# Kernel tuning notes

Hardware: AMD Instinct MI355X
Metric: run time of the kernel (lower is better)

The kernel has to match this reference:

```python
import jax, jax.numpy as jnp
import numpy as np


def _resize_axis(x, axis, n_out):
    # trilinear (per-axis linear) resize, matching torch align_corners=False
    n_in = x.shape[axis]
    coords = jnp.clip((jnp.arange(n_out) + 0.5) * (n_in / n_out) - 0.5, 0.0, n_in - 1)
    lo = jnp.floor(coords).astype(jnp.int32)
    hi = jnp.minimum(lo + 1, n_in - 1)
    w = (coords - lo).astype(x.dtype)
    shp = [1] * x.ndim
    shp[axis] = n_out
    w = w.reshape(shp)
    return jnp.take(x, lo, axis=axis) * (1 - w) + jnp.take(x, hi, axis=axis) * w


def setup_inputs() -> dict:
    key = jax.random.key(0)
    ks = jax.random.split(key, 16)
    M, B, C, H, W, Z = 4, 1, 64, 64, 64, 64
    mini = max(C // 32, 4)  # = 4
    s = 0.05
    return {
        'modalities': jax.random.normal(ks[0], (M, B, C, H, W, Z), jnp.float32),
        'wq1': jax.random.normal(ks[1], (mini, C), jnp.float32) * s,
        'bq1': jax.random.normal(ks[2], (mini,), jnp.float32) * s,
        'wq2': jax.random.normal(ks[3], (2, mini), jnp.float32) * s,
        'bq2': jax.random.normal(ks[4], (2,), jnp.float32) * s,
        'wa1': jax.random.normal(ks[5], (mini, C), jnp.float32) * s,
        'ba1': jax.random.normal(ks[6], (mini,), jnp.float32) * s,
        'wa2': jax.random.normal(ks[7], (1, mini), jnp.float32) * s,
        'ba2': jax.random.normal(ks[8], (1,), jnp.float32) * s,
        'wf': jax.random.normal(ks[9], (C, C), jnp.float32) * s,
        'bf': jax.random.normal(ks[10], (C,), jnp.float32) * s,
        'wg1': jax.random.normal(ks[11], (mini, C), jnp.float32) * s,
        'bg1': jax.random.normal(ks[12], (mini,), jnp.float32) * s,
        'wg2': jax.random.normal(ks[13], (C, mini), jnp.float32) * s,
        'bg2': jax.random.normal(ks[14], (C,), jnp.float32) * s,
    }


def reference(modalities, wq1, bq1, wq2, bq2, wa1, ba1, wa2, ba2, wf, bf, wg1, bg1, wg2, bg2):
    M, B, C, H, W, Z = modalities.shape
    x = modalities
    # quality net: GAP -> 1x1 conv -> relu -> 1x1 conv -> sigmoid (all 1x1x1 convs == matmuls)
    gap = x.mean(axis=(3, 4, 5))  # [M,B,C]
    scores = jax.nn.sigmoid(jnp.maximum(gap @ wq1.T + bq1, 0.0) @ wq2.T + bq2)  # [M,B,2]
    qw = scores.mean(axis=2)      # quality_weight per modality, [M,B] (mean over ch+unit spatial)
    t = qw.mean(axis=1)           # scalar weight contribution per modality, [M]
    # cross attention: adaptive avg pool to 4^3, tiny MLP, trilinear upsample back to H,W,Z
    d = x.reshape(M, B, C, 4, H // 4, 4, W // 4, 4, Z // 4).mean(axis=(4, 6, 8))  # [M,B,C,4,4,4]
    h = jnp.maximum(jnp.einsum('mbcxyz,kc->mbkxyz', d, wa1) + ba1.reshape(1, 1, -1, 1, 1, 1), 0.0)
    a = jax.nn.sigmoid(jnp.einsum('mbkxyz,ok->mboxyz', h, wa2) + ba2.reshape(1, 1, -1, 1, 1, 1))
    a = _resize_axis(_resize_axis(_resize_axis(a, 3, H), 4, W), 5, Z)  # [M,B,1,H,W,Z]
    # pairwise aggregation: enhancement_i = sum_{j!=i} x_j * attn_j * qw_j, normalized by sum_{j!=i} t_j
    contrib = x * a * qw[:, :, None, None, None, None]  # [M,B,C,H,W,Z]
    S = contrib.sum(axis=0, keepdims=True)
    T = t.sum()
    enh = (S - contrib) / (T - t)[:, None, None, None, None, None]
    # fusion 1x1 conv + gate
    fused = jnp.einsum('mbchwz,dc->mbdhwz', enh, wf) + bf.reshape(1, 1, -1, 1, 1, 1)
    g = fused.mean(axis=(3, 4, 5))  # [M,B,C]
    gate = jax.nn.sigmoid(jnp.maximum(g @ wg1.T + bg1, 0.0) @ wg2.T + bg2)  # [M,B,C]
    enhanced = x + gate[:, :, :, None, None, None] * fused
    boundary = scores[:, :, 0].reshape(M, B, 1, 1, 1, 1)
    semantic = scores[:, :, 1].reshape(M, B, 1, 1, 1, 1)
    return enhanced, boundary, semantic
```

## Files before the change

### kernel.cpp

```cpp
#include <hip/hip_runtime.h>
#include <math.h>

typedef __attribute__((ext_vector_type(4))) float f4;
typedef __attribute__((ext_vector_type(8))) short s8v;
typedef __attribute__((ext_vector_type(4))) unsigned int u4v;
typedef __attribute__((ext_vector_type(2))) unsigned int u2v;

#define NVOX 262144
#define MB_TOT 67108864

__device__ __forceinline__ float sigm(float x){ return 1.0f/(1.0f+expf(-x)); }
__device__ __forceinline__ unsigned short f2b(float f){
  unsigned x = __float_as_uint(f);
  return (unsigned short)((x + 0x7fffu + ((x>>16)&1u)) >> 16);
}
__device__ __forceinline__ unsigned cvtpk(float lo, float hi){
  unsigned r;
  asm("v_cvt_pk_bf16_f32 %0, %1, %2" : "=v"(r) : "v"(lo), "v"(hi));
  return r;
}
__device__ __forceinline__ float bl(unsigned u){ return __uint_as_float(u<<16); }
__device__ __forceinline__ float bh(unsigned u){ return __uint_as_float(u & 0xffff0000u); }


#define LD(I,J) (*reinterpret_cast<const f4*>(xp + (size_t)((I)*64 + (J))*64 + chunk*4))

#define BODY(I, V) { \
  float s_ = ((V).x+(V).y)+((V).z+(V).w); \
  float wB_ = (V).x*wqz0 + (V).y*wqz1 + (V).z*wqz2 + (V).w*wqz3; \
  float wA_ = s_ - wB_; \
  bacc += s_; \
  const int   li_  = ((I)<8)?0:(((I)>=56)?3:(((I)-8)>>4)); \
  const float wi_  = ((I)<8||(I)>=56)?0.0f:(((I)+0.5f)*0.0625f-0.5f-(float)li_); \
  const float h0_ = (li_==0)?(1.0f-wi_):0.0f; \
  const float h1_ = (li_==1)?(1.0f-wi_):((li_==0)?wi_:0.0f); \
  const float h2_ = (li_==2)?(1.0f-wi_):((li_==1)?wi_:0.0f); \
  const float h3_ = (li_==3)?(1.0f-wi_):((li_==2)?wi_:0.0f); \
  float eA_ = cjA*wA_, eB_ = cjA*wB_, fA_ = cjB*wA_, fB_ = cjB*wB_; \
  if (h0_ != 0.0f){ a0A0 += h0_*eA_; a0A1 += h0_*eB_; a0B0 += h0_*fA_; a0B1 += h0_*fB_; } \
  if (h1_ != 0.0f){ a1A0 += h1_*eA_; a1A1 += h1_*eB_; a1B0 += h1_*fA_; a1B1 += h1_*fB_; } \
  if (h2_ != 0.0f){ a2A0 += h2_*eA_; a2A1 += h2_*eB_; a2B0 += h2_*fA_; a2B1 += h2_*fB_; } \
  if (h3_ != 0.0f){ a3A0 += h3_*eA_; a3A1 += h3_*eB_; a3B0 += h3_*fA_; a3B1 += h3_*fB_; } \
}

#define SEG16(I0) \
  _Pragma("unroll") \
  for (int ib=0; ib<16; ib+=4){ \
    f4 v0_ = LD((I0)+ib+0, j); \
    f4 v1_ = LD((I0)+ib+1, j); \
    f4 v2_ = LD((I0)+ib+2, j); \
    f4 v3_ = LD((I0)+ib+3, j); \
    BODY((I0)+ib+0, v0_); \
    BODY((I0)+ib+1, v1_); \
    BODY((I0)+ib+2, v2_); \
    BODY((I0)+ib+3, v3_); \
  }

__global__ __launch_bounds__(512) void k_pass1(const float* __restrict__ x,
                                               float* __restrict__ dsums,
                                               float* __restrict__ xbsums){
  __shared__ float xbL[64];
  __shared__ float bsL[64];
  int tid = threadIdx.x;
  int b = blockIdx.x;
  int mc  = b >> 2;
  int seg = b & 3;
  if (tid < 64){ xbL[tid]=0.f; bsL[tid]=0.f; }
  __syncthreads();
  const float* xp = x + (size_t)mc * NVOX;
  int chunk = tid & 15;
  int jbase = tid >> 4;
  float wqz0,wqz1,wqz2,wqz3;
  {
    int z0 = chunk*4;
    int lzc0 = (z0<8)?0:((z0>=56)?3:((z0-8)>>4));
    wqz0 = (z0  <8||z0  >=56)?0.0f:((z0+0.5f)*0.0625f-0.5f-(float)lzc0);
    wqz1 = (z0+1<8||z0+1>=56)?0.0f:((z0+1.5f)*0.0625f-0.5f-(float)lzc0);
    wqz2 = (z0+2<8||z0+2>=56)?0.0f:((z0+2.5f)*0.0625f-0.5f-(float)lzc0);
    wqz3 = (z0+3<8||z0+3>=56)?0.0f:((z0+3.5f)*0.0625f-0.5f-(float)lzc0);
  }
  int lzc = (chunk*4<8)?0:((chunk*4>=56)?3:((chunk*4-8)>>4));
  int kq = chunk >> 2;

#pragma unroll
  for (int jh=0; jh<2; ++jh){
    int j = jbase + jh*32;
    float cjA, cjB; int lj;
    {
      float cj = fminf(fmaxf((j+0.5f)*0.0625f-0.5f, 0.0f), 3.0f);
      lj = (int)cj; float wj = cj - (float)lj;
      cjA = 1.0f - wj; cjB = wj;
    }
    float a0A0=0.f,a0A1=0.f,a0B0=0.f,a0B1=0.f;
    float a1A0=0.f,a1A1=0.f,a1B0=0.f,a1B1=0.f;
    float a2A0=0.f,a2A1=0.f,a2B0=0.f,a2B1=0.f;
    float a3A0=0.f,a3A1=0.f,a3B0=0.f,a3B1=0.f;
    float bacc=0.f;

    if      (seg == 0){ SEG16(0)  }
    else if (seg == 1){ SEG16(16) }
    else if (seg == 2){ SEG16(32) }
    else              { SEG16(48) }

    {
      int p00 = lj*4 + lzc;
      atomicAdd(&xbL[ 0 + p00], a0A0);
      atomicAdd(&xbL[16 + p00], a1A0);
      atomicAdd(&xbL[32 + p00], a2A0);
      atomicAdd(&xbL[48 + p00], a3A0);
      if (lzc < 3){
        atomicAdd(&xbL[ 0 + p00+1], a0A1);
        atomicAdd(&xbL[16 + p00+1], a1A1);
        atomicAdd(&xbL[32 + p00+1], a2A1);
        atomicAdd(&xbL[48 + p00+1], a3A1);
      }
      if (lj < 3){
        atomicAdd(&xbL[ 0 + p00+4], a0B0);
        atomicAdd(&xbL[16 + p00+4], a1B0);
        atomicAdd(&xbL[32 + p00+4], a2B0);
        atomicAdd(&xbL[48 + p00+4], a3B0);
        if (lzc < 3){
          atomicAdd(&xbL[ 0 + p00+5], a0B1);
          atomicAdd(&xbL[16 + p00+5], a1B1);
          atomicAdd(&xbL[32 + p00+5], a2B1);
          atomicAdd(&xbL[48 + p00+5], a3B1);
        }
      }
      atomicAdd(&bsL[seg*16 + (j>>4)*4 + kq], bacc);
    }
  }
  __syncthreads();
  if (tid < 64){
    atomicAdd(&xbsums[(size_t)mc*64 + tid], xbL[tid]);
    atomicAdd(&dsums [(size_t)mc*64 + tid], bsL[tid]);
  }
}

__global__ __launch_bounds__(256) void k_pass2(
    const float* __restrict__ dsums, const float* __restrict__ xbsums,
    const float* __restrict__ wq1, const float* __restrict__ bq1,
    const float* __restrict__ wq2, const float* __restrict__ bq2,
    const float* __restrict__ wa1, const float* __restrict__ ba1,
    const float* __restrict__ wa2, const float* __restrict__ ba2,
    const float* __restrict__ wf,  const float* __restrict__ bfv,
    const float* __restrict__ wg1, const float* __restrict__ bg1,
    const float* __restrict__ wg2, const float* __restrict__ bg2,
    float* __restrict__ wsa, float* __restrict__ wsgate,
    float* __restrict__ wsqw, float* __restrict__ wsinv,
    unsigned short* __restrict__ wfb,
    float* __restrict__ outp)
{
  __shared__ float sGap[256];
  __shared__ float sA[256];
  __shared__ float sCm[256];
  __shared__ float sG[256];
  __shared__ float sGG[16];
  __shared__ float sQw[4];
  int tid = threadIdx.x;
  int m = tid>>6, c = tid&63;
  for (int t = tid; t < 4096; t += 256) wfb[t] = f2b(wf[t]);
  {
    float s=0.f;
    const float* dp = dsums + (size_t)tid*64;
    for (int p=0;p<64;++p) s += dp[p];
    sGap[tid] = s * (1.0f/262144.0f);
  }
  {
    int p = c;
    float h0=0,h1=0,h2=0,h3=0;
    for (int cc=0; cc<64; ++cc){
      float dm = dsums[((size_t)(m*64+cc))*64+p] * (1.0f/4096.0f);
      h0 += dm * wa1[0*64+cc];
      h1 += dm * wa1[1*64+cc];
      h2 += dm * wa1[2*64+cc];
      h3 += dm * wa1[3*64+cc];
    }
    h0 = fmaxf(h0 + ba1[0], 0.f);
    h1 = fmaxf(h1 + ba1[1], 0.f);
    h2 = fmaxf(h2 + ba1[2], 0.f);
    h3 = fmaxf(h3 + ba1[3], 0.f);
    float s = h0*wa2[0] + h1*wa2[1] + h2*wa2[2] + h3*wa2[3] + ba2[0];
    float aa = sigm(s);
    sA[tid] = aa;
    wsa[tid] = aa;
  }
  __syncthreads();
  if (tid < 4){
    int mm = tid;
    float q0=0,q1=0,q2=0,q3=0;
    for (int cc=0; cc<64; ++cc){
      float g = sGap[mm*64+cc];
      q0 += g*wq1[0*64+cc];
      q1 += g*wq1[1*64+cc];
      q2 += g*wq1[2*64+cc];
      q3 += g*wq1[3*64+cc];
    }
    q0 = fmaxf(q0+bq1[0],0.f); q1 = fmaxf(q1+bq1[1],0.f);
    q2 = fmaxf(q2+bq1[2],0.f); q3 = fmaxf(q3+bq1[3],0.f);
    float s0 = sigm(q0*wq2[0]+q1*wq2[1]+q2*wq2[2]+q3*wq2[3]+bq2[0]);
    float s1 = sigm(q0*wq2[4]+q1*wq2[5]+q2*wq2[6]+q3*wq2[7]+bq2[1]);
    sQw[mm] = 0.5f*(s0+s1);
    outp[MB_TOT + mm]     = s0;
    outp[MB_TOT + 4 + mm] = s1;
  }
  __syncthreads();
  float qw_m = sQw[m];
  float T = sQw[0]+sQw[1]+sQw[2]+sQw[3];
  float inv_m = 1.0f/(T - qw_m);
  if (tid < 4){ wsqw[tid] = sQw[tid]; wsinv[tid] = 1.0f/(T - sQw[tid]); }
  {
    const float* xbp = xbsums + (size_t)tid*64;
    float s=0.f;
    for (int p=0;p<64;++p) s += sA[m*64+p]*xbp[p];
    sCm[tid] = qw_m * s * (1.0f/262144.0f);
  }
  __syncthreads();
  {
    int dd = c;
    float acc=0.f;
    for (int cc=0; cc<64; ++cc){
      float Sm = sCm[0*64+cc]+sCm[1*64+cc]+sCm[2*64+cc]+sCm[3*64+cc];
      float em = (Sm - sCm[m*64+cc]) * inv_m;
      acc += em * wf[dd*64+cc];
    }
    sG[tid] = acc + bfv[dd];
  }
  __syncthreads();
  if (tid < 16){
    int mm = tid>>2, k = tid&3;
    float acc=0.f;
    for (int dd=0; dd<64; ++dd) acc += sG[mm*64+dd]*wg1[k*64+dd];
    sGG[tid] = fmaxf(acc + bg1[k], 0.f);
  }
  __syncthreads();
  {
    float s = sGG[m*4+0]*wg2[c*4+0] + sGG[m*4+1]*wg2[c*4+1]
            + sGG[m*4+2]*wg2[c*4+2] + sGG[m*4+3]*wg2[c*4+3] + bg2[c];
    wsgate[tid] = sigm(s);
  }
}

__global__ __launch_bounds__(256) void k_pass3(
    const float* __restrict__ x, const unsigned short* __restrict__ wfb,
    const float* __restrict__ bfv,
    const float* __restrict__ wsa, const float* __restrict__ wsgate,
    const float* __restrict__ wsqw, const float* __restrict__ wsinv,
    float* __restrict__ outp)
{
  __shared__ unsigned int xt[4][32][68];
  __shared__ unsigned int fusedT[64][34];
  __shared__ float aCell[4][64];
  __shared__ float gateL[4][64];
  __shared__ __align__(16) float auq[4][64];
  __shared__ float bfL[64];
  __shared__ float A2[4][4];
  int tid = threadIdx.x;
  int b = 4095 - (int)blockIdx.x;
  int i = b >> 6, j = b & 63;
  size_t V0 = (size_t)b * 64;
  int w    = tid >> 6;
  int lane = tid & 63;
  int ks   = lane >> 4;
  int r    = lane & 15;
  int vox16 = w << 4;

  const float* xw = x + (size_t)(w*64)*NVOX + V0 + r*4;
  f4 v[16];
#pragma unroll
  for (int rr=0; rr<16; ++rr){
    int cc = ks*16 + rr;
    v[rr] = *reinterpret_cast<const f4*>(xw + (size_t)cc*NVOX);
  }
  aCell[w][lane] = wsa[tid];
  gateL[w][lane] = wsgate[tid];
  if (tid < 64) bfL[tid] = bfv[tid];
#pragma unroll
  for (int rr=0; rr<16; rr+=2){
    u4v pk;
#pragma unroll
    for (int q=0;q<4;++q) pk[q] = cvtpk(v[rr][q], v[rr+1][q]);
    *reinterpret_cast<u4v*>(&xt[w][ks*8 + (rr>>1)][r*4]) = pk;
  }
  __syncthreads();

  if (tid < 16){
    int mm = tid>>2, pz = tid&3;
    float ci = fminf(fmaxf((i+0.5f)*0.0625f-0.5f,0.f),3.f);
    int li=(int)ci; float wi=ci-(float)li; int hiI=li<3?li+1:3;
    float cj = fminf(fmaxf((j+0.5f)*0.0625f-0.5f,0.f),3.f);
    int lj=(int)cj; float wj=cj-(float)lj; int hj=lj<3?lj+1:3;
    A2[mm][pz] = (1.f-wi)*((1.f-wj)*aCell[mm][li*16+lj*4+pz] + wj*aCell[mm][li*16+hj*4+pz])
               + wi*((1.f-wj)*aCell[mm][hiI*16+lj*4+pz] + wj*aCell[mm][hiI*16+hj*4+pz]);
  }
  __syncthreads();
  {
    int mm = tid>>6, z = tid&63;
    float cz = fminf(fmaxf((z+0.5f)*0.0625f-0.5f,0.f),3.f);
    int lz=(int)cz; float wzf=cz-(float)lz; int hz=lz<3?lz+1:3;
    auq[mm][z] = ((1.f-wzf)*A2[mm][lz] + wzf*A2[mm][hz]) * wsqw[mm];
  }
  __syncthreads();

  s8v bfr[4][2];
#pragma unroll
  for (int t=0;t<4;++t)
#pragma unroll
    for (int kk=0;kk<2;++kk)
      bfr[t][kk] = *reinterpret_cast<const s8v*>(&wfb[(t*16 + r)*64 + kk*32 + ks*8]);

  f4 acc[4][4];
#pragma unroll
  for (int mm=0;mm<4;++mm)
#pragma unroll
    for (int t=0;t<4;++t) acc[mm][t] = f4{0.f,0.f,0.f,0.f};

#pragma unroll
  for (int mm=0;mm<4;++mm){
    union { unsigned int u[4]; s8v s; } A0, A1;
#pragma unroll
    for (int q=0;q<4;++q){
      A0.u[q] = xt[mm][ks*4+q][vox16+r];
      A1.u[q] = xt[mm][16+ks*4+q][vox16+r];
    }
#pragma unroll
    for (int t=0;t<4;++t){
      acc[mm][t] = __builtin_amdgcn_mfma_f32_16x16x32_bf16(A0.s, bfr[t][0], acc[mm][t], 0,0,0);
      acc[mm][t] = __builtin_amdgcn_mfma_f32_16x16x32_bf16(A1.s, bfr[t][1], acc[mm][t], 0,0,0);
    }
  }

  f4 aq[4]; float invv[4];
#pragma unroll
  for (int mm=0;mm<4;++mm){
    aq[mm]  = *reinterpret_cast<const f4*>(&auq[mm][vox16 + 4*ks]);
    invv[mm] = wsinv[mm];
  }
  f4 FS[4];
#pragma unroll
  for (int t=0;t<4;++t){
    FS[t] = f4{0.f,0.f,0.f,0.f};
#pragma unroll
    for (int mm=0;mm<4;++mm)
#pragma unroll
      for (int q=0;q<4;++q) FS[t][q] += aq[mm][q]*acc[mm][t][q];
  }

  int g4 = tid >> 4;
  int r4l = tid & 15;
#pragma unroll
  for (int mm=0;mm<4;++mm){
#pragma unroll
    for (int t=0;t<4;++t){
      int dd = t*16 + r;
      float bfvv = bfL[dd];
      float f0 = (FS[t][0] - aq[mm][0]*acc[mm][t][0])*invv[mm] + bfvv;
      float f1 = (FS[t][1] - aq[mm][1]*acc[mm][t][1])*invv[mm] + bfvv;
      float f2 = (FS[t][2] - aq[mm][2]*acc[mm][t][2])*invv[mm] + bfvv;
      float f3 = (FS[t][3] - aq[mm][3]*acc[mm][t][3])*invv[mm] + bfvv;
      u2v pk2;
      pk2.x = cvtpk(f0, f1);
      pk2.y = cvtpk(f2, f3);
      *reinterpret_cast<u2v*>(&fusedT[dd][(vox16 + ks*4)>>1]) = pk2;
    }
    __syncthreads();
#pragma unroll
    for (int rr=0; rr<4; ++rr){
      int dd = rr*16 + g4;
      float g = gateL[mm][dd];
      u4v xu = *reinterpret_cast<const u4v*>(&xt[mm][dd>>1][r4l*4]);
      u2v fu = *reinterpret_cast<const u2v*>(&fusedT[dd][r4l*2]);
      f4 o;
      float x0 = (dd&1) ? bh(xu[0]) : bl(xu[0]);
      float x1 = (dd&1) ? bh(xu[1]) : bl(xu[1]);
      float x2 = (dd&1) ? bh(xu[2]) : bl(xu[2]);
      float x3 = (dd&1) ? bh(xu[3]) : bl(xu[3]);
      o[0] = x0 + g*bl(fu.x);
      o[1] = x1 + g*bh(fu.x);
      o[2] = x2 + g*bl(fu.y);
      o[3] = x3 + g*bh(fu.y);
      *reinterpret_cast<f4*>(outp + (size_t)(mm*64+dd)*NVOX + V0 + r4l*4) = o;
    }
    __syncthreads();
  }
}

extern "C" void kernel_launch(void* const* d_in, const int* in_sizes, int n_in,
                              void* d_out, int out_size, void* d_ws, size_t ws_size,
                              hipStream_t stream){
  const float* x   = (const float*)d_in[0];
  const float* wq1 = (const float*)d_in[1];
  const float* bq1 = (const float*)d_in[2];
  const float* wq2 = (const float*)d_in[3];
  const float* bq2 = (const float*)d_in[4];
  const float* wa1 = (const float*)d_in[5];
  const float* ba1 = (const float*)d_in[6];
  const float* wa2 = (const float*)d_in[7];
  const float* ba2 = (const float*)d_in[8];
  const float* wf  = (const float*)d_in[9];
  const float* bfv = (const float*)d_in[10];
  const float* wg1 = (const float*)d_in[11];
  const float* bg1 = (const float*)d_in[12];
  const float* wg2 = (const float*)d_in[13];
  const float* bg2 = (const float*)d_in[14];
  float* outp = (float*)d_out;
  float* w = (float*)d_ws;
  float* dsums  = w;
  float* xbsums = w + 16384;
  float* wsa    = w + 32768;
  float* wsgate = w + 33024;
  float* wsqw   = w + 33280;
  float* wsinv  = w + 33284;
  unsigned short* wfb = (unsigned short*)(w + 33288);
  hipMemsetAsync(w, 0, 32768*sizeof(float), stream);
  hipLaunchKernelGGL(k_pass1, dim3(1024), dim3(512), 0, stream, x, dsums, xbsums);
  hipLaunchKernelGGL(k_pass2, dim3(1), dim3(256), 0, stream, dsums, xbsums,
                     wq1,bq1,wq2,bq2,wa1,ba1,wa2,ba2,wf,bfv,wg1,bg1,wg2,bg2,
                     wsa, wsgate, wsqw, wsinv, wfb, outp);
  hipLaunchKernelGGL(k_pass3, dim3(4096), dim3(256), 0, stream, x, wfb, bfv,
                     wsa, wsgate, wsqw, wsinv, outp);
}
```

Measured before the change: 246.4 us.

## Cache a bf16 copy of the input in pass1 for the pass3 matmul

```diff
diff --git a/kernel.cpp b/kernel.cpp
--- a/kernel.cpp
+++ b/kernel.cpp
@@ -24,6 +24,11 @@
 
 
 #define LD(I,J) (*reinterpret_cast<const f4*>(xp + (size_t)((I)*64 + (J))*64 + chunk*4))
+
+#define ST16(I, V) if (use16){ \
+  u2v pk_; pk_.x = cvtpk((V).x,(V).y); pk_.y = cvtpk((V).z,(V).w); \
+  *reinterpret_cast<u2v*>(xbo + (size_t)((I)*64 + j)*32) = pk_; \
+}
 
 #define BODY(I, V) { \
   float s_ = ((V).x+(V).y)+((V).z+(V).w); \
@@ -43,22 +48,26 @@
   if (h3_ != 0.0f){ a3A0 += h3_*eA_; a3A1 += h3_*eB_; a3B0 += h3_*fA_; a3B1 += h3_*fB_; } \
 }
 
-#define SEG16(I0) \
-  _Pragma("unroll") \
-  for (int ib=0; ib<16; ib+=4){ \
-    f4 v0_ = LD((I0)+ib+0, j); \
-    f4 v1_ = LD((I0)+ib+1, j); \
-    f4 v2_ = LD((I0)+ib+2, j); \
-    f4 v3_ = LD((I0)+ib+3, j); \
-    BODY((I0)+ib+0, v0_); \
-    BODY((I0)+ib+1, v1_); \
-    BODY((I0)+ib+2, v2_); \
-    BODY((I0)+ib+3, v3_); \
-  }
+#define SEG8(I0) { \
+  f4 v0_ = LD((I0)+0, j); \
+  f4 v1_ = LD((I0)+1, j); \
+  f4 v2_ = LD((I0)+2, j); \
+  f4 v3_ = LD((I0)+3, j); \
+  f4 v4_ = LD((I0)+4, j); \
+  f4 v5_ = LD((I0)+5, j); \
+  f4 v6_ = LD((I0)+6, j); \
+  f4 v7_ = LD((I0)+7, j); \
+  ST16((I0)+0, v0_); ST16((I0)+1, v1_); ST16((I0)+2, v2_); ST16((I0)+3, v3_); \
+  ST16((I0)+4, v4_); ST16((I0)+5, v5_); ST16((I0)+6, v6_); ST16((I0)+7, v7_); \
+  BODY((I0)+0, v0_); BODY((I0)+1, v1_); BODY((I0)+2, v2_); BODY((I0)+3, v3_); \
+  BODY((I0)+4, v4_); BODY((I0)+5, v5_); BODY((I0)+6, v6_); BODY((I0)+7, v7_); \
+}
 
 __global__ __launch_bounds__(512) void k_pass1(const float* __restrict__ x,
                                                float* __restrict__ dsums,
-                                               float* __restrict__ xbsums){
+                                               float* __restrict__ xbsums,
+                                               unsigned* __restrict__ xb16u,
+                                               int use16){
   __shared__ float xbL[64];
   __shared__ float bsL[64];
   int tid = threadIdx.x;
@@ -82,9 +91,10 @@
   int lzc = (chunk*4<8)?0:((chunk*4>=56)?3:((chunk*4-8)>>4));
   int kq = chunk >> 2;
 
-#pragma unroll
+#pragma unroll 1
   for (int jh=0; jh<2; ++jh){
     int j = jbase + jh*32;
+    unsigned* xbo = xb16u + (size_t)mc*(NVOX/2) + chunk*2;
     float cjA, cjB; int lj;
     {
       float cj = fminf(fmaxf((j+0.5f)*0.0625f-0.5f, 0.0f), 3.0f);
@@ -97,10 +107,10 @@
     float a3A0=0.f,a3A1=0.f,a3B0=0.f,a3B1=0.f;
     float bacc=0.f;
 
-    if      (seg == 0){ SEG16(0)  }
-    else if (seg == 1){ SEG16(16) }
-    else if (seg == 2){ SEG16(32) }
-    else              { SEG16(48) }
+    if      (seg == 0){ SEG8(0)  SEG8(8)  }
+    else if (seg == 1){ SEG8(16) SEG8(24) }
+    else if (seg == 2){ SEG8(32) SEG8(40) }
+    else              { SEG8(48) SEG8(56) }
 
     {
       int p00 = lj*4 + lzc;
@@ -241,11 +251,12 @@
 }
 
 __global__ __launch_bounds__(256) void k_pass3(
-    const float* __restrict__ x, const unsigned short* __restrict__ wfb,
+    const float* __restrict__ x, const unsigned* __restrict__ xb16u,
+    const unsigned short* __restrict__ wfb,
     const float* __restrict__ bfv,
     const float* __restrict__ wsa, const float* __restrict__ wsgate,
     const float* __restrict__ wsqw, const float* __restrict__ wsinv,
-    float* __restrict__ outp)
+    float* __restrict__ outp, int use16)
 {
   __shared__ unsigned int xt[4][32][68];
   __shared__ unsigned int fusedT[64][34];
@@ -264,22 +275,46 @@
   int r    = lane & 15;
   int vox16 = w << 4;
 
-  const float* xw = x + (size_t)(w*64)*NVOX + V0 + r*4;
-  f4 v[16];
-#pragma unroll
-  for (int rr=0; rr<16; ++rr){
-    int cc = ks*16 + rr;
-    v[rr] = *reinterpret_cast<const f4*>(xw + (size_t)cc*NVOX);
-  }
   aCell[w][lane] = wsa[tid];
   gateL[w][lane] = wsgate[tid];
   if (tid < 64) bfL[tid] = bfv[tid];
-#pragma unroll
-  for (int rr=0; rr<16; rr+=2){
-    u4v pk;
-#pragma unroll
-    for (int q=0;q<4;++q) pk[q] = cvtpk(v[rr][q], v[rr+1][q]);
-    *reinterpret_cast<u4v*>(&xt[w][ks*8 + (rr>>1)][r*4]) = pk;
+
+  if (use16){
+    int ks8 = lane >> 3;
+    int r8  = lane & 7;
+    const unsigned* xsrc = xb16u + ((size_t)(w*64)*NVOX + V0)/2 + r8*4;
+#pragma unroll
+    for (int rr=0; rr<8; rr+=2){
+      int cc = ks8*8 + rr;
+      u4v a  = *reinterpret_cast<const u4v*>(xsrc + (size_t)cc*(NVOX/2));
+      u4v bq = *reinterpret_cast<const u4v*>(xsrc + (size_t)(cc+1)*(NVOX/2));
+      u4v w0, w1;
+#pragma unroll
+      for (int k=0;k<2;++k){
+        w0[2*k]   = (a[k] & 0xffffu) | (bq[k] << 16);
+        w0[2*k+1] = (a[k] >> 16)     | (bq[k] & 0xffff0000u);
+        w1[2*k]   = (a[k+2] & 0xffffu) | (bq[k+2] << 16);
+        w1[2*k+1] = (a[k+2] >> 16)     | (bq[k+2] & 0xffff0000u);
+      }
+      int cc2 = ks8*4 + (rr>>1);
+      *reinterpret_cast<u4v*>(&xt[w][cc2][r8*8])   = w0;
+      *reinterpret_cast<u4v*>(&xt[w][cc2][r8*8+4]) = w1;
+    }
+  } else {
+    const float* xw = x + (size_t)(w*64)*NVOX + V0 + r*4;
+    f4 v[16];
+#pragma unroll
+    for (int rr=0; rr<16; ++rr){
+      int cc = ks*16 + rr;
+      v[rr] = *reinterpret_cast<const f4*>(xw + (size_t)cc*NVOX);
+    }
+#pragma unroll
+    for (int rr=0; rr<16; rr+=2){
+      u4v pk;
+#pragma unroll
+      for (int q=0;q<4;++q) pk[q] = cvtpk(v[rr][q], v[rr+1][q]);
+      *reinterpret_cast<u4v*>(&xt[w][ks*8 + (rr>>1)][r*4]) = pk;
+    }
   }
   __syncthreads();
 
@@ -411,11 +446,14 @@
   float* wsqw   = w + 33280;
   float* wsinv  = w + 33284;
   unsigned short* wfb = (unsigned short*)(w + 33288);
+  unsigned* xb16u = (unsigned*)(w + 35336);
+  size_t need = ((size_t)35336 + 33554432) * 4;
+  int use16 = (ws_size >= need) ? 1 : 0;
   hipMemsetAsync(w, 0, 32768*sizeof(float), stream);
-  hipLaunchKernelGGL(k_pass1, dim3(1024), dim3(512), 0, stream, x, dsums, xbsums);
+  hipLaunchKernelGGL(k_pass1, dim3(1024), dim3(512), 0, stream, x, dsums, xbsums, xb16u, use16);
   hipLaunchKernelGGL(k_pass2, dim3(1), dim3(256), 0, stream, dsums, xbsums,
                      wq1,bq1,wq2,bq2,wa1,ba1,wa2,ba2,wf,bfv,wg1,bg1,wg2,bg2,
                      wsa, wsgate, wsqw, wsinv, wfb, outp);
-  hipLaunchKernelGGL(k_pass3, dim3(4096), dim3(256), 0, stream, x, wfb, bfv,
-                     wsa, wsgate, wsqw, wsinv, outp);
-}
+  hipLaunchKernelGGL(k_pass3, dim3(4096), dim3(256), 0, stream, x, xb16u, wfb, bfv,
+                     wsa, wsgate, wsqw, wsinv, outp, use16);
+}
```

Measured after the change: 259.5 us. 5.3% more time.
